# Kernel tuning notes

Hardware: AMD Instinct MI355X
Metric: run time of the kernel (lower is better)

The kernel has to match this reference:

```python
import jax, jax.numpy as jnp
import numpy as np

EPS = 1e-6
B, DIM, H, W = 2, 128, 64, 64
HEADS, DH = 4, 64            # dim_head = dim // heads * 2
INNER = HEADS * DH           # 256


def _dwsep(x, dw, pw):
    """depthwise 3x3 (groups=C, SAME) followed by 1x1 pointwise. x: [b,C,h,w]."""
    C = x.shape[1]
    y = jax.lax.conv_general_dilated(x, dw, (1, 1), 'SAME',
                                     feature_group_count=C,
                                     dimension_numbers=('NCHW', 'OIHW', 'NCHW'))
    return jnp.einsum('bchw,oc->bohw', y, pw)


def _head_ln(x, w, b):
    """per-head LayerNorm over last dim. x: [b,heads,N,dh]; w,b: [heads,dh]."""
    mu = x.mean(-1, keepdims=True)
    var = jnp.mean((x - mu) ** 2, -1, keepdims=True)
    return (x - mu) * jax.lax.rsqrt(var + EPS) * w[None, :, None, :] + b[None, :, None, :]


def setup_inputs() -> dict:
    key = jax.random.key(0)
    ks = jax.random.split(key, 8)
    s = 0.02
    return {
        'x': jax.random.normal(ks[0], (B, DIM, H, W), jnp.float32),
        'pe_w': jax.random.normal(ks[1], (DIM, 2), jnp.float32) * s,   # 1x1 conv coords->dim
        'pe_b': jnp.zeros((DIM,), jnp.float32),
        'qkv_dw': jax.random.normal(ks[2], (DIM, 1, 3, 3), jnp.float32) * s,
        'qkv_pw': jax.random.normal(ks[3], (3 * INNER, DIM), jnp.float32) * s,
        'out_dw': jax.random.normal(ks[4], (INNER, 1, 3, 3), jnp.float32) * s,
        'out_pw': jax.random.normal(ks[5], (DIM, INNER), jnp.float32) * s,
        'nq_w': jnp.ones((HEADS, DH), jnp.float32), 'nq_b': jnp.zeros((HEADS, DH), jnp.float32),
        'nk_w': jnp.ones((HEADS, DH), jnp.float32), 'nk_b': jnp.zeros((HEADS, DH), jnp.float32),
        'no_w': jnp.ones((HEADS, DH), jnp.float32), 'no_b': jnp.zeros((HEADS, DH), jnp.float32),
        'ln_w': jnp.ones((DIM,), jnp.float32), 'ln_b': jnp.zeros((DIM,), jnp.float32),
    }


def reference(x, pe_w, pe_b, qkv_dw, qkv_pw, out_dw, out_pw,
              nq_w, nq_b, nk_w, nk_b, no_w, no_b, ln_w, ln_b):
    b, c, h, w = x.shape
    heads, dh = nq_w.shape
    n = h * w

    # Euclidean positional encoding: linspace mesh [2,h,w] -> 1x1 conv -> add
    gx = jnp.linspace(0.0, 1.0, h)
    gy = jnp.linspace(0.0, 1.0, w)
    mesh = jnp.stack(jnp.meshgrid(gx, gy, indexing='ij'), 0)          # [2,h,w]
    pos = jnp.einsum('chw,dc->dhw', mesh, pe_w) + pe_b[:, None, None]
    x = x + pos[None]

    # QKV via depthwise-separable conv
    qkv = _dwsep(x, qkv_dw, qkv_pw)                                   # [b,3*inner,h,w]
    q, k, v = jnp.split(qkv, 3, axis=1)

    def to_heads(t):  # 'b (dim_head heads) h w -> b heads (h w) dim_head'
        return t.reshape(b, dh, heads, n).transpose(0, 2, 3, 1)

    q, k, v = map(to_heads, (q, k, v))                                # [b,heads,n,dh]
    q = _head_ln(q, nq_w, nq_b)
    k = _head_ln(k, nk_w, nk_b)

    attn = jnp.einsum('bhid,bhjd->bhij', q, k) * (dh ** -0.5)
    attn = jax.nn.softmax(attn, axis=-1)
    out = jnp.einsum('bhij,bhjd->bhid', attn, v)
    out = out + v                                                      # skip connection
    out = _head_ln(out, no_w, no_b)

    # 'b heads (h w) dim_head -> b (dim_head heads) h w'
    out = out.transpose(0, 3, 1, 2).reshape(b, dh * heads, h, w)
    out = _dwsep(out, out_dw, out_pw)                                  # [b,dim,h,w]

    # LayerNorm2d over channel dim at each spatial position
    mu = out.mean(1, keepdims=True)
    var = jnp.mean((out - mu) ** 2, 1, keepdims=True)
    out = (out - mu) * jax.lax.rsqrt(var + EPS)
    out = out * ln_w[None, :, None, None] + ln_b[None, :, None, None]
    return out
```

## Files before the change

kernel.cpp:

```cpp
#include <hip/hip_runtime.h>

#define BB 2
#define NTOK 4096
#define DIM 128
#define INNER 256
#define HEADS 4
#define DH 64
#define QS 0.18033688011112043f

typedef unsigned short u16;
typedef __attribute__((ext_vector_type(8))) short bf16x8;
typedef __attribute__((ext_vector_type(16))) float f32x16;

__device__ inline unsigned f2bf1(float f) {
  union { float f; unsigned u; } a; a.f = f;
  return (a.u + 0x7fffu + ((a.u >> 16) & 1u)) >> 16;
}
__device__ inline unsigned packbf(float lo, float hi) {
  return f2bf1(lo) | (f2bf1(hi) << 16);
}
__device__ inline float bf2f(u16 h) {
  union { unsigned u; float f; } a; a.u = ((unsigned)h) << 16;
  return a.f;
}
__device__ inline unsigned cvtpk(float lo, float hi) {
  unsigned r;
  asm("v_cvt_pk_bf16_f32 %0, %1, %2" : "=v"(r) : "v"(lo), "v"(hi));
  return r;
}

template <int C, bool PE>
__global__ __launch_bounds__(256) void k_dwconv(const float* __restrict__ x,
    const float* __restrict__ pew, const float* __restrict__ peb,
    const float* __restrict__ dw, u16* __restrict__ out) {
  constexpr int CG = C / 16;
  __shared__ float ld[16][640];
  int bid = blockIdx.x;
  int strip = bid & 7;
  int cg = (bid >> 3) % CG;
  int b = bid / (8 * CG);
  int r0 = strip * 8;
  int t = threadIdx.x;
#pragma unroll
  for (int c = 0; c < 16; ++c) {
    int gc = cg * 16 + c;
    const float* xb = x + ((size_t)(b * C + gc)) * NTOK;
    float s0 = 0.f, s1 = 0.f, pb = 0.f;
    if (PE) {
      s0 = pew[gc * 2] * (1.f / 63.f);
      s1 = pew[gc * 2 + 1] * (1.f / 63.f);
      pb = peb[gc];
    }
#pragma unroll
    for (int u = 0; u < 3; ++u) {
      int pos = t + 256 * u;
      if (pos < 640) {
        int rr = r0 - 1 + (pos >> 6);
        int col = pos & 63;
        float v = 0.f;
        if ((unsigned)rr < 64u) {
          v = xb[rr * 64 + col];
          if (PE) v += rr * s0 + col * s1 + pb;
        }
        ld[c][pos] = v;
      }
    }
  }
  __syncthreads();
  float accv[2][16];
#pragma unroll
  for (int c = 0; c < 16; ++c) {
    const float* wp = dw + (cg * 16 + c) * 9;
    float w0 = wp[0], w1 = wp[1], w2 = wp[2], w3 = wp[3], w4 = wp[4];
    float w5 = wp[5], w6 = wp[6], w7 = wp[7], w8 = wp[8];
#pragma unroll
    for (int pp = 0; pp < 2; ++pp) {
      int p = t + 256 * pp;
      int lr = (p >> 6) + 1;
      int j = p & 63;
      const float* rm = &ld[c][(lr - 1) * 64];
      const float* rc = &ld[c][lr * 64];
      const float* rp = &ld[c][(lr + 1) * 64];
      float acc = rm[j] * w1 + rc[j] * w4 + rp[j] * w7;
      if (j > 0)  acc += rm[j - 1] * w0 + rc[j - 1] * w3 + rp[j - 1] * w6;
      if (j < 63) acc += rm[j + 1] * w2 + rc[j + 1] * w5 + rp[j + 1] * w8;
      accv[pp][c] = acc;
    }
  }
#pragma unroll
  for (int pp = 0; pp < 2; ++pp) {
    int p = t + 256 * pp;
    unsigned ow[8];
#pragma unroll
    for (int q = 0; q < 8; ++q) ow[q] = packbf(accv[pp][2 * q], accv[pp][2 * q + 1]);
    u16* ob = out + ((size_t)(b * NTOK) + strip * 512 + p) * C + cg * 16;
    *(uint4*)(ob) = *(uint4*)&ow[0];
    *(uint4*)(ob + 8) = *(uint4*)&ow[4];
  }
}

__global__ __launch_bounds__(256) void k_gemm_qkv(
    const float* __restrict__ W, const u16* __restrict__ Yb,
    float* __restrict__ q_o, float* __restrict__ k_o, u16* __restrict__ v_t) {
  __shared__ u16 Wl[128 * 64];
  __shared__ u16 Yl[128 * 64];
  int gid = blockIdx.x;
  int nt = gid & 31;
  int mt = (gid >> 5) % 6;
  int b = gid / 192;
  int t = threadIdx.x;
  int w = t >> 6, l = t & 63;
  int wm = w >> 1, wn = w & 1;
  int hi = l >> 5, lq = l & 31;

  f32x16 acc[2][2];
#pragma unroll
  for (int fm = 0; fm < 2; ++fm)
#pragma unroll
    for (int fn = 0; fn < 2; ++fn)
#pragma unroll
      for (int r = 0; r < 16; ++r) acc[fm][fn][r] = 0.f;

  const float* Wbase = W + (size_t)(mt * 128) * 128;
  const u16* Ybase = Yb + ((size_t)(b * NTOK) + nt * 128) * 128;

  for (int k0 = 0; k0 < 128; k0 += 64) {
#pragma unroll
    for (int u = 0; u < 4; ++u) {
      int gI = t + 256 * u;
      int row = gI >> 3, g = gI & 7;
      float4 f0 = *(const float4*)(Wbase + (size_t)row * 128 + k0 + g * 8);
      float4 f1 = *(const float4*)(Wbase + (size_t)row * 128 + k0 + g * 8 + 4);
      uint4 uu;
      uu.x = cvtpk(f0.x, f0.y); uu.y = cvtpk(f0.z, f0.w);
      uu.z = cvtpk(f1.x, f1.y); uu.w = cvtpk(f1.z, f1.w);
      *(uint4*)&Wl[row * 64 + 8 * (g ^ (row & 7))] = uu;
      uint4 yv = *(const uint4*)(Ybase + (size_t)row * 128 + k0 + g * 8);
      *(uint4*)&Yl[row * 64 + 8 * (g ^ (row & 7))] = yv;
    }
    __syncthreads();
#pragma unroll
    for (int ks = 0; ks < 4; ++ks) {
      bf16x8 aF[2], bF[2];
#pragma unroll
      for (int fm = 0; fm < 2; ++fm) {
        int row = wm * 64 + fm * 32 + lq;
        aF[fm] = *(bf16x8*)&Wl[row * 64 + 8 * ((2 * ks + hi) ^ (row & 7))];
      }
#pragma unroll
      for (int fn = 0; fn < 2; ++fn) {
        int row = wn * 64 + fn * 32 + lq;
        bF[fn] = *(bf16x8*)&Yl[row * 64 + 8 * ((2 * ks + hi) ^ (row & 7))];
      }
#pragma unroll
      for (int fm = 0; fm < 2; ++fm)
#pragma unroll
        for (int fn = 0; fn < 2; ++fn)
          acc[fm][fn] = __builtin_amdgcn_mfma_f32_32x32x16_bf16(
              aF[fm], bF[fn], acc[fm][fn], 0, 0, 0);
    }
    __syncthreads();
  }

#pragma unroll
  for (int fm = 0; fm < 2; ++fm)
#pragma unroll
    for (int fn = 0; fn < 2; ++fn)
#pragma unroll
      for (int reg = 0; reg < 16; ++reg) {
        int rl = (reg & 3) + 8 * (reg >> 2) + 4 * hi;
        int o = mt * 128 + wm * 64 + fm * 32 + rl;
        int n = nt * 128 + wn * 64 + fn * 32 + lq;
        float val = acc[fm][fn][reg];
        int part = o >> 8, rr = o & 255;
        int head = rr & 3, d = rr >> 2;
        size_t idx = ((size_t)(b * HEADS + head) * DH + d) * NTOK + n;
        if (part == 0) q_o[idx] = val;
        else if (part == 1) k_o[idx] = val;
        else v_t[idx] = (u16)f2bf1(val);
      }
}

__global__ __launch_bounds__(256) void k_lnqk_t(const float* __restrict__ qh,
    const float* __restrict__ kh, u16* __restrict__ qo, u16* __restrict__ ko,
    const float* __restrict__ nqw, const float* __restrict__ nqb,
    const float* __restrict__ nkw, const float* __restrict__ nkb) {
  __shared__ float ld[64][65];
  int bh = blockIdx.x >> 6, nt = blockIdx.x & 63;
  int head = bh & 3;
  int n0 = nt * 64;
  int t = threadIdx.x;
  int dg = t & 3, nn = t >> 2;
  int dl = t >> 4, nc = t & 15;
#pragma unroll
  for (int m = 0; m < 2; ++m) {
    const float* src = (m ? kh : qh) + ((size_t)bh * DH) * NTOK + n0;
    const float* wp = (m ? nkw : nqw) + head * DH;
    const float* bp = (m ? nkb : nqb) + head * DH;
    u16* dst = (m ? ko : qo) + ((size_t)bh * NTOK + n0) * DH;
    if (m) __syncthreads();
#pragma unroll
    for (int pass = 0; pass < 4; ++pass) {
      int d = pass * 16 + dl;
      *(float4*)&ld[d][nc * 4] = *(const float4*)(src + (size_t)d * NTOK + nc * 4);
    }
    __syncthreads();
    float s1 = 0.f, s2 = 0.f;
#pragma unroll
    for (int i = 0; i < 16; ++i) {
      float v = ld[dg * 16 + i][nn];
      s1 += v; s2 += v * v;
    }
    s1 += __shfl_xor(s1, 1); s2 += __shfl_xor(s2, 1);
    s1 += __shfl_xor(s1, 2); s2 += __shfl_xor(s2, 2);
    float mu = s1 * (1.f / 64.f);
    float var = s2 * (1.f / 64.f) - mu * mu;
    float ri = rsqrtf(var + 1e-6f);
    float sc = m ? 1.f : QS;
    unsigned ow[8];
#pragma unroll
    for (int i = 0; i < 8; ++i) {
      int d0 = dg * 16 + 2 * i;
      float y0 = ((ld[d0][nn] - mu) * ri * wp[d0] + bp[d0]) * sc;
      float y1 = ((ld[d0 + 1][nn] - mu) * ri * wp[d0 + 1] + bp[d0 + 1]) * sc;
      ow[i] = packbf(y0, y1);
    }
    *(uint4*)(dst + (size_t)nn * DH + dg * 16) = *(uint4*)&ow[0];
    *(uint4*)(dst + (size_t)nn * DH + dg * 16 + 8) = *(uint4*)&ow[4];
  }
}

__global__ __launch_bounds__(512, 4) void k_attn4(
    const u16* __restrict__ qb, const u16* __restrict__ kb,
    const u16* __restrict__ vtb, const float* __restrict__ now,
    const float* __restrict__ nob, float* __restrict__ att) {
  __shared__ __align__(16) u16 kvbuf[16384];
  __shared__ float mlm[256], mll[256];
  __shared__ float nw[DH], nb[DH];
  const int bh = blockIdx.x >> 6, qt = blockIdx.x & 63;
  const int b = bh >> 2, head = bh & 3;
  const int t = threadIdx.x;
  const int w = t >> 6, l = t & 63;
  const int qg = w & 1, h = w >> 1;
  const int hi = l >> 5, lq = l & 31;
  if (t < DH) { nw[t] = now[head * DH + t]; nb[t] = nob[head * DH + t]; }

  const int q0 = qt * 64 + qg * 32;
  const u16* qrow = qb + (size_t)(bh * NTOK + q0 + lq) * DH;
  bf16x8 qf[4];
#pragma unroll
  for (int ks = 0; ks < 4; ++ks)
    qf[ks] = *(const bf16x8*)(qrow + 16 * ks + 8 * hi);

  const int st = t & 127;
  const int KQs = h * 4096, VQs = h * 4096 + 2048;
  const u16* kbase = kb + (size_t)(bh * NTOK) * DH;
  const u16* vbase = vtb + (size_t)(bh * DH) * NTOK;
  uint4 kr0, kr1, vr0, vr1;
  const int krow = st >> 3, kg = st & 7;
  const int vrow = st >> 2, vg = st & 3;

  auto loadTile = [&](int s) {
    int kv0 = h * 1024 + s * 32;
    kr0 = *(const uint4*)(kbase + (size_t)(kv0 + krow) * DH + kg * 8);
    kr1 = *(const uint4*)(kbase + (size_t)(kv0 + krow + 16) * DH + kg * 8);
    vr0 = *(const uint4*)(vbase + (size_t)vrow * NTOK + kv0 + vg * 8);
    vr1 = *(const uint4*)(vbase + (size_t)(vrow + 32) * NTOK + kv0 + vg * 8);
  };
  loadTile(0);

  f32x16 oT0, oT1;
#pragma unroll
  for (int i = 0; i < 16; ++i) { oT0[i] = 0.f; oT1[i] = 0.f; }
  float m_s = -1e30f, l_s = 0.f;
  const u16* KL = kvbuf + KQs;
  const u16* VL = kvbuf + VQs;

  for (int s = 0; s < 32; ++s) {
    __syncthreads();
    *(uint4*)&kvbuf[KQs + krow * 64 + 8 * (kg ^ (krow & 7))] = kr0;
    *(uint4*)&kvbuf[KQs + (krow + 16) * 64 + 8 * (kg ^ ((krow + 16) & 7))] = kr1;
    *(uint4*)&kvbuf[VQs + vrow * 32 + 8 * (vg ^ ((vrow >> 1) & 3))] = vr0;
    *(uint4*)&kvbuf[VQs + (vrow + 32) * 32 + 8 * (vg ^ (((vrow + 32) >> 1) & 3))] = vr1;
    __syncthreads();
    if (s < 31) loadTile(s + 1);

    f32x16 sT;
#pragma unroll
    for (int i = 0; i < 16; ++i) sT[i] = 0.f;
#pragma unroll
    for (int ks = 0; ks < 4; ++ks) {
      bf16x8 a = *(bf16x8*)&KL[lq * 64 + 8 * ((2 * ks + hi) ^ (lq & 7))];
      sT = __builtin_amdgcn_mfma_f32_32x32x16_bf16(a, qf[ks], sT, 0, 0, 0);
    }
    float mo = sT[0];
#pragma unroll
    for (int i = 1; i < 16; ++i) mo = fmaxf(mo, sT[i]);
    mo = fmaxf(mo, __shfl_xor(mo, 32));
    float mn = fmaxf(m_s, mo);
    if (!__all(mn - m_s <= 8.0f)) {
      float alpha = exp2f(m_s - mn);
      m_s = mn;
      l_s *= alpha;
#pragma unroll
      for (int i = 0; i < 16; ++i) { oT0[i] *= alpha; oT1[i] *= alpha; }
    }
    unsigned pw[8];
    float rs = 0.f;
#pragma unroll
    for (int j = 0; j < 8; ++j) {
      float e0 = exp2f(sT[2 * j] - m_s);
      float e1 = exp2f(sT[2 * j + 1] - m_s);
      rs += e0 + e1;
      pw[j] = cvtpk(e0, e1);
    }
    rs += __shfl_xor(rs, 32);
    l_s += rs;
    bf16x8 pf[2];
#pragma unroll
    for (int ks = 0; ks < 2; ++ks) {
      unsigned z0 = hi ? pw[4 * ks] : pw[4 * ks + 2];
      unsigned z1 = hi ? pw[4 * ks + 1] : pw[4 * ks + 3];
      unsigned r0 = (unsigned)__shfl_xor((int)z0, 32);
      unsigned r1 = (unsigned)__shfl_xor((int)z1, 32);
      union { unsigned u[4]; bf16x8 v; } U;
      if (hi) { U.u[0] = r0; U.u[1] = r1; U.u[2] = pw[4 * ks + 2]; U.u[3] = pw[4 * ks + 3]; }
      else    { U.u[0] = pw[4 * ks]; U.u[1] = pw[4 * ks + 1]; U.u[2] = r0; U.u[3] = r1; }
      pf[ks] = U.v;
    }
#pragma unroll
    for (int ks = 0; ks < 2; ++ks) {
      bf16x8 v0 = *(bf16x8*)&VL[lq * 32 + 8 * ((2 * ks + hi) ^ ((lq >> 1) & 3))];
      bf16x8 v1 = *(bf16x8*)&VL[(32 + lq) * 32 + 8 * ((2 * ks + hi) ^ (((32 + lq) >> 1) & 3))];
      oT0 = __builtin_amdgcn_mfma_f32_32x32x16_bf16(v0, pf[ks], oT0, 0, 0, 0);
      oT1 = __builtin_amdgcn_mfma_f32_32x32x16_bf16(v1, pf[ks], oT1, 0, 0, 0);
    }
  }

  float* mrg = (float*)kvbuf;
  __syncthreads();
  if (h >= 2) {
    float* mg = mrg + ((h - 2) * 2 + qg) * 2048;
#pragma unroll
    for (int i = 0; i < 16; ++i) {
      mg[i * 64 + l] = oT0[i];
      mg[(16 + i) * 64 + l] = oT1[i];
    }
    mlm[((h - 2) * 2 + qg) * 64 + l] = m_s;
    mll[((h - 2) * 2 + qg) * 64 + l] = l_s;
  }
  __syncthreads();
  if (h < 2) {
    int slot = h * 2 + qg;
    const float* mg = mrg + slot * 2048;
    float m1 = mlm[slot * 64 + l], l1 = mll[slot * 64 + l];
    float M = fmaxf(m_s, m1);
    float a0 = exp2f(m_s - M), a1 = exp2f(m1 - M);
#pragma unroll
    for (int i = 0; i < 16; ++i) {
      oT0[i] = oT0[i] * a0 + mg[i * 64 + l] * a1;
      oT1[i] = oT1[i] * a0 + mg[(16 + i) * 64 + l] * a1;
    }
    l_s = l_s * a0 + l1 * a1;
    m_s = M;
  }
  __syncthreads();
  if (h == 1) {
    float* mg = mrg + qg * 2048;
#pragma unroll
    for (int i = 0; i < 16; ++i) {
      mg[i * 64 + l] = oT0[i];
      mg[(16 + i) * 64 + l] = oT1[i];
    }
    mlm[qg * 64 + l] = m_s;
    mll[qg * 64 + l] = l_s;
  }
  __syncthreads();
  if (h == 0) {
    const float* mg = mrg + qg * 2048;
    float m1 = mlm[qg * 64 + l], l1 = mll[qg * 64 + l];
    float M = fmaxf(m_s, m1);
    float a0 = exp2f(m_s - M), a1 = exp2f(m1 - M);
    float L = l_s * a0 + l1 * a1;
    float inv = 1.f / L;
    float ov[32];
#pragma unroll
    for (int i = 0; i < 16; ++i) {
      ov[i] = (oT0[i] * a0 + mg[i * 64 + l] * a1) * inv;
      ov[16 + i] = (oT1[i] * a0 + mg[(16 + i) * 64 + l] * a1) * inv;
    }
    int n = q0 + lq;
#pragma unroll
    for (int dt = 0; dt < 2; ++dt)
#pragma unroll
      for (int g = 0; g < 4; ++g)
#pragma unroll
        for (int r = 0; r < 4; ++r) {
          int d = dt * 32 + g * 8 + hi * 4 + r;
          ov[dt * 16 + g * 4 + r] +=
              bf2f(vtb[((size_t)(bh * DH) + d) * NTOK + n]);
        }
    float s1 = 0.f, s2 = 0.f;
#pragma unroll
    for (int i = 0; i < 32; ++i) { s1 += ov[i]; s2 += ov[i] * ov[i]; }
    s1 += __shfl_xor(s1, 32);
    s2 += __shfl_xor(s2, 32);
    float mu = s1 * (1.f / 64.f);
    float va = s2 * (1.f / 64.f) - mu * mu;
    float ri = rsqrtf(va + 1e-6f);
    float* ob = att + (size_t)b * INNER * NTOK + n;
#pragma unroll
    for (int dt = 0; dt < 2; ++dt)
#pragma unroll
      for (int g = 0; g < 4; ++g)
#pragma unroll
        for (int r = 0; r < 4; ++r) {
          int d = dt * 32 + g * 8 + hi * 4 + r;
          float y = (ov[dt * 16 + g * 4 + r] - mu) * ri * nw[d] + nb[d];
          ob[(size_t)(d * 4 + head) * NTOK] = y;
        }
  }
}

__global__ __launch_bounds__(256) void k_gemm_ln(
    const float* __restrict__ W, const u16* __restrict__ Yb,
    const float* __restrict__ lnw, const float* __restrict__ lnb,
    float* __restrict__ out) {
  __shared__ u16 Wl[128 * 64];
  __shared__ u16 Yl[64 * 64];
  __shared__ float red[256];
  int gid = blockIdx.x;
  int nt = gid & 63;
  int b = gid >> 6;
  int t = threadIdx.x;
  int w = t >> 6, l = t & 63;
  int wm = w >> 1, wn = w & 1;
  int hi = l >> 5, lq = l & 31;

  f32x16 acc[2];
#pragma unroll
  for (int fm = 0; fm < 2; ++fm)
#pragma unroll
    for (int r = 0; r < 16; ++r) acc[fm][r] = 0.f;

  const u16* Ybase = Yb + ((size_t)(b * NTOK) + nt * 64) * INNER;

  for (int k0 = 0; k0 < 256; k0 += 64) {
#pragma unroll
    for (int u = 0; u < 4; ++u) {
      int gI = t + 256 * u;
      int row = gI >> 3, g = gI & 7;
      float4 f0 = *(const float4*)(W + (size_t)row * 256 + k0 + g * 8);
      float4 f1 = *(const float4*)(W + (size_t)row * 256 + k0 + g * 8 + 4);
      uint4 uu;
      uu.x = cvtpk(f0.x, f0.y); uu.y = cvtpk(f0.z, f0.w);
      uu.z = cvtpk(f1.x, f1.y); uu.w = cvtpk(f1.z, f1.w);
      *(uint4*)&Wl[row * 64 + 8 * (g ^ (row & 7))] = uu;
    }
#pragma unroll
    for (int u = 0; u < 2; ++u) {
      int gI = t + 256 * u;
      int row = gI >> 3, g = gI & 7;
      uint4 yv = *(const uint4*)(Ybase + (size_t)row * 256 + k0 + g * 8);
      *(uint4*)&Yl[row * 64 + 8 * (g ^ (row & 7))] = yv;
    }
    __syncthreads();
#pragma unroll
    for (int ks = 0; ks < 4; ++ks) {
      bf16x8 aF[2], bF;
#pragma unroll
      for (int fm = 0; fm < 2; ++fm) {
        int row = wm * 64 + fm * 32 + lq;
        aF[fm] = *(bf16x8*)&Wl[row * 64 + 8 * ((2 * ks + hi) ^ (row & 7))];
      }
      {
        int row = wn * 32 + lq;
        bF = *(bf16x8*)&Yl[row * 64 + 8 * ((2 * ks + hi) ^ (row & 7))];
      }
#pragma unroll
      for (int fm = 0; fm < 2; ++fm)
        acc[fm] = __builtin_amdgcn_mfma_f32_32x32x16_bf16(aF[fm], bF, acc[fm], 0, 0, 0);
    }
    __syncthreads();
  }

  float s1 = 0.f, s2 = 0.f;
#pragma unroll
  for (int fm = 0; fm < 2; ++fm)
#pragma unroll
    for (int r = 0; r < 16; ++r) {
      float v = acc[fm][r];
      s1 += v; s2 += v * v;
    }
  s1 += __shfl_xor(s1, 32);
  s2 += __shfl_xor(s2, 32);
  int col = wn * 32 + lq;
  if (hi == 0) { red[wm * 128 + col] = s1; red[wm * 128 + 64 + col] = s2; }
  __syncthreads();
  float t1 = red[col] + red[128 + col];
  float t2 = red[64 + col] + red[192 + col];
  float mu = t1 * (1.f / 128.f);
  float var = t2 * (1.f / 128.f) - mu * mu;
  float ri = rsqrtf(var + 1e-6f);
  int n = nt * 64 + col;
  float* ob = out + (size_t)b * DIM * NTOK + n;
#pragma unroll
  for (int fm = 0; fm < 2; ++fm)
#pragma unroll
    for (int r = 0; r < 16; ++r) {
      int m = wm * 64 + fm * 32 + (r & 3) + 8 * (r >> 2) + 4 * hi;
      float y = (acc[fm][r] - mu) * ri * lnw[m] + lnb[m];
      ob[(size_t)m * NTOK] = y;
    }
}

extern "C" void kernel_launch(void* const* d_in, const int* in_sizes, int n_in,
                              void* d_out, int out_size, void* d_ws,
                              size_t ws_size, hipStream_t stream) {
  const float* x      = (const float*)d_in[0];
  const float* pe_w   = (const float*)d_in[1];
  const float* pe_b   = (const float*)d_in[2];
  const float* qkv_dw = (const float*)d_in[3];
  const float* qkv_pw = (const float*)d_in[4];
  const float* out_dw = (const float*)d_in[5];
  const float* out_pw = (const float*)d_in[6];
  const float* nq_w   = (const float*)d_in[7];
  const float* nq_b   = (const float*)d_in[8];
  const float* nk_w   = (const float*)d_in[9];
  const float* nk_b   = (const float*)d_in[10];
  const float* no_w   = (const float*)d_in[11];
  const float* no_b   = (const float*)d_in[12];
  const float* ln_w   = (const float*)d_in[13];
  const float* ln_b   = (const float*)d_in[14];

  float* ws = (float*)d_ws;
  u16*   dwyb = (u16*)ws;
  float* qhb  = ws + (1u << 19);
  float* khb  = ws + (1u << 19) + (1u << 21);
  u16*   vtb  = (u16*)(ws + (1u << 19) + (2u << 21));
  u16*   qbb  = (u16*)(ws + (1u << 19) + (2u << 21) + (1u << 20));
  u16*   kbb  = (u16*)(ws + (1u << 19) + (2u << 21) + (2u << 20));
  float* att  = qhb;
  u16*   db16 = (u16*)khb;
  float* outp = (float*)d_out;

  k_dwconv<DIM, true><<<dim3(128), dim3(256), 0, stream>>>(
      x, pe_w, pe_b, qkv_dw, dwyb);
  k_gemm_qkv<<<dim3(BB * 6 * 32), dim3(256), 0, stream>>>(
      qkv_pw, dwyb, qhb, khb, vtb);
  k_lnqk_t<<<dim3(512), dim3(256), 0, stream>>>(
      qhb, khb, qbb, kbb, nq_w, nq_b, nk_w, nk_b);
  k_attn4<<<dim3(512), dim3(512), 0, stream>>>(qbb, kbb, vtb, no_w, no_b, att);
  k_dwconv<INNER, false><<<dim3(256), dim3(256), 0, stream>>>(
      att, nullptr, nullptr, out_dw, db16);
  k_gemm_ln<<<dim3(BB * 64), dim3(256), 0, stream>>>(
      out_pw, db16, ln_w, ln_b, outp);
}
```

Before: 223.3 us.

## Load attention K/V fragments directly from global and halve dwconv strips

The attention kernel no longer stages K/V tiles through shared memory with barriers. Each of the four waves loads its MFMA operands straight from global memory (through cache) for its own KV quarter, and a block now covers 32 queries with 256 threads, giving twice as many blocks. The final merge combines the three partial softmax states sequentially in wave 0. The depthwise conv kernels now process 4-row strips, doubling their grid size. This removes per-iteration syncs and LDS traffic, at the cost of uncoalesced per-lane global loads for K/V and a heavier serial merge.

```diff
diff --git a/kernel.cpp b/kernel.cpp
--- a/kernel.cpp
+++ b/kernel.cpp
@@ -34,12 +34,12 @@
     const float* __restrict__ pew, const float* __restrict__ peb,
     const float* __restrict__ dw, u16* __restrict__ out) {
   constexpr int CG = C / 16;
-  __shared__ float ld[16][640];
+  __shared__ float ld[16][384];
   int bid = blockIdx.x;
-  int strip = bid & 7;
-  int cg = (bid >> 3) % CG;
-  int b = bid / (8 * CG);
-  int r0 = strip * 8;
+  int strip = bid & 15;
+  int cg = (bid >> 4) % CG;
+  int b = bid / (16 * CG);
+  int r0 = strip * 4;
   int t = threadIdx.x;
 #pragma unroll
   for (int c = 0; c < 16; ++c) {
@@ -52,9 +52,9 @@
       pb = peb[gc];
     }
 #pragma unroll
-    for (int u = 0; u < 3; ++u) {
+    for (int u = 0; u < 2; ++u) {
       int pos = t + 256 * u;
-      if (pos < 640) {
+      if (pos < 384) {
         int rr = r0 - 1 + (pos >> 6);
         int col = pos & 63;
         float v = 0.f;
@@ -67,36 +67,26 @@
     }
   }
   __syncthreads();
-  float accv[2][16];
+  int lr = (t >> 6) + 1;
+  int j = t & 63;
+  float res[16];
 #pragma unroll
   for (int c = 0; c < 16; ++c) {
     const float* wp = dw + (cg * 16 + c) * 9;
-    float w0 = wp[0], w1 = wp[1], w2 = wp[2], w3 = wp[3], w4 = wp[4];
-    float w5 = wp[5], w6 = wp[6], w7 = wp[7], w8 = wp[8];
-#pragma unroll
-    for (int pp = 0; pp < 2; ++pp) {
-      int p = t + 256 * pp;
-      int lr = (p >> 6) + 1;
-      int j = p & 63;
-      const float* rm = &ld[c][(lr - 1) * 64];
-      const float* rc = &ld[c][lr * 64];
-      const float* rp = &ld[c][(lr + 1) * 64];
-      float acc = rm[j] * w1 + rc[j] * w4 + rp[j] * w7;
-      if (j > 0)  acc += rm[j - 1] * w0 + rc[j - 1] * w3 + rp[j - 1] * w6;
-      if (j < 63) acc += rm[j + 1] * w2 + rc[j + 1] * w5 + rp[j + 1] * w8;
-      accv[pp][c] = acc;
-    }
-  }
-#pragma unroll
-  for (int pp = 0; pp < 2; ++pp) {
-    int p = t + 256 * pp;
-    unsigned ow[8];
-#pragma unroll
-    for (int q = 0; q < 8; ++q) ow[q] = packbf(accv[pp][2 * q], accv[pp][2 * q + 1]);
-    u16* ob = out + ((size_t)(b * NTOK) + strip * 512 + p) * C + cg * 16;
-    *(uint4*)(ob) = *(uint4*)&ow[0];
-    *(uint4*)(ob + 8) = *(uint4*)&ow[4];
-  }
+    const float* rm = &ld[c][(lr - 1) * 64];
+    const float* rc = &ld[c][lr * 64];
+    const float* rp = &ld[c][(lr + 1) * 64];
+    float acc = rm[j] * wp[1] + rc[j] * wp[4] + rp[j] * wp[7];
+    if (j > 0)  acc += rm[j - 1] * wp[0] + rc[j - 1] * wp[3] + rp[j - 1] * wp[6];
+    if (j < 63) acc += rm[j + 1] * wp[2] + rc[j + 1] * wp[5] + rp[j + 1] * wp[8];
+    res[c] = acc;
+  }
+  unsigned ow[8];
+#pragma unroll
+  for (int q = 0; q < 8; ++q) ow[q] = packbf(res[2 * q], res[2 * q + 1]);
+  u16* ob = out + ((size_t)(b * NTOK) + strip * 256 + t) * C + cg * 16;
+  *(uint4*)(ob) = *(uint4*)&ow[0];
+  *(uint4*)(ob + 8) = *(uint4*)&ow[4];
 }
 
 __global__ __launch_bounds__(256) void k_gemm_qkv(
@@ -230,67 +220,43 @@
   }
 }
 
-__global__ __launch_bounds__(512, 4) void k_attn4(
+__global__ __launch_bounds__(256, 4) void k_attn5(
     const u16* __restrict__ qb, const u16* __restrict__ kb,
     const u16* __restrict__ vtb, const float* __restrict__ now,
     const float* __restrict__ nob, float* __restrict__ att) {
-  __shared__ __align__(16) u16 kvbuf[16384];
-  __shared__ float mlm[256], mll[256];
+  __shared__ float mrg[3][2048];
+  __shared__ float mstore[3][64], lstore[3][64];
   __shared__ float nw[DH], nb[DH];
-  const int bh = blockIdx.x >> 6, qt = blockIdx.x & 63;
+  const int bh = blockIdx.x >> 7, qt = blockIdx.x & 127;
   const int b = bh >> 2, head = bh & 3;
   const int t = threadIdx.x;
-  const int w = t >> 6, l = t & 63;
-  const int qg = w & 1, h = w >> 1;
+  const int h = t >> 6, l = t & 63;
   const int hi = l >> 5, lq = l & 31;
   if (t < DH) { nw[t] = now[head * DH + t]; nb[t] = nob[head * DH + t]; }
 
-  const int q0 = qt * 64 + qg * 32;
+  const int q0 = qt * 32;
   const u16* qrow = qb + (size_t)(bh * NTOK + q0 + lq) * DH;
   bf16x8 qf[4];
 #pragma unroll
   for (int ks = 0; ks < 4; ++ks)
     qf[ks] = *(const bf16x8*)(qrow + 16 * ks + 8 * hi);
 
-  const int st = t & 127;
-  const int KQs = h * 4096, VQs = h * 4096 + 2048;
-  const u16* kbase = kb + (size_t)(bh * NTOK) * DH;
-  const u16* vbase = vtb + (size_t)(bh * DH) * NTOK;
-  uint4 kr0, kr1, vr0, vr1;
-  const int krow = st >> 3, kg = st & 7;
-  const int vrow = st >> 2, vg = st & 3;
-
-  auto loadTile = [&](int s) {
-    int kv0 = h * 1024 + s * 32;
-    kr0 = *(const uint4*)(kbase + (size_t)(kv0 + krow) * DH + kg * 8);
-    kr1 = *(const uint4*)(kbase + (size_t)(kv0 + krow + 16) * DH + kg * 8);
-    vr0 = *(const uint4*)(vbase + (size_t)vrow * NTOK + kv0 + vg * 8);
-    vr1 = *(const uint4*)(vbase + (size_t)(vrow + 32) * NTOK + kv0 + vg * 8);
-  };
-  loadTile(0);
+  const u16* krow = kb + ((size_t)(bh * NTOK) + h * 1024 + lq) * DH;
+  const u16* vrow0 = vtb + ((size_t)(bh * DH) + lq) * NTOK + h * 1024;
+  const u16* vrow1 = vtb + ((size_t)(bh * DH) + 32 + lq) * NTOK + h * 1024;
 
   f32x16 oT0, oT1;
 #pragma unroll
   for (int i = 0; i < 16; ++i) { oT0[i] = 0.f; oT1[i] = 0.f; }
   float m_s = -1e30f, l_s = 0.f;
-  const u16* KL = kvbuf + KQs;
-  const u16* VL = kvbuf + VQs;
 
   for (int s = 0; s < 32; ++s) {
-    __syncthreads();
-    *(uint4*)&kvbuf[KQs + krow * 64 + 8 * (kg ^ (krow & 7))] = kr0;
-    *(uint4*)&kvbuf[KQs + (krow + 16) * 64 + 8 * (kg ^ ((krow + 16) & 7))] = kr1;
-    *(uint4*)&kvbuf[VQs + vrow * 32 + 8 * (vg ^ ((vrow >> 1) & 3))] = vr0;
-    *(uint4*)&kvbuf[VQs + (vrow + 32) * 32 + 8 * (vg ^ (((vrow + 32) >> 1) & 3))] = vr1;
-    __syncthreads();
-    if (s < 31) loadTile(s + 1);
-
     f32x16 sT;
 #pragma unroll
     for (int i = 0; i < 16; ++i) sT[i] = 0.f;
 #pragma unroll
     for (int ks = 0; ks < 4; ++ks) {
-      bf16x8 a = *(bf16x8*)&KL[lq * 64 + 8 * ((2 * ks + hi) ^ (lq & 7))];
+      bf16x8 a = *(const bf16x8*)(krow + (size_t)s * 32 * DH + 16 * ks + 8 * hi);
       sT = __builtin_amdgcn_mfma_f32_32x32x16_bf16(a, qf[ks], sT, 0, 0, 0);
     }
     float mo = sT[0];
@@ -330,65 +296,43 @@
     }
 #pragma unroll
     for (int ks = 0; ks < 2; ++ks) {
-      bf16x8 v0 = *(bf16x8*)&VL[lq * 32 + 8 * ((2 * ks + hi) ^ ((lq >> 1) & 3))];
-      bf16x8 v1 = *(bf16x8*)&VL[(32 + lq) * 32 + 8 * ((2 * ks + hi) ^ (((32 + lq) >> 1) & 3))];
+      bf16x8 v0 = *(const bf16x8*)(vrow0 + s * 32 + 16 * ks + 8 * hi);
+      bf16x8 v1 = *(const bf16x8*)(vrow1 + s * 32 + 16 * ks + 8 * hi);
       oT0 = __builtin_amdgcn_mfma_f32_32x32x16_bf16(v0, pf[ks], oT0, 0, 0, 0);
       oT1 = __builtin_amdgcn_mfma_f32_32x32x16_bf16(v1, pf[ks], oT1, 0, 0, 0);
     }
   }
 
-  float* mrg = (float*)kvbuf;
   __syncthreads();
-  if (h >= 2) {
-    float* mg = mrg + ((h - 2) * 2 + qg) * 2048;
+  if (h > 0) {
+    float* mg = mrg[h - 1];
 #pragma unroll
     for (int i = 0; i < 16; ++i) {
       mg[i * 64 + l] = oT0[i];
       mg[(16 + i) * 64 + l] = oT1[i];
     }
-    mlm[((h - 2) * 2 + qg) * 64 + l] = m_s;
-    mll[((h - 2) * 2 + qg) * 64 + l] = l_s;
-  }
-  __syncthreads();
-  if (h < 2) {
-    int slot = h * 2 + qg;
-    const float* mg = mrg + slot * 2048;
-    float m1 = mlm[slot * 64 + l], l1 = mll[slot * 64 + l];
-    float M = fmaxf(m_s, m1);
-    float a0 = exp2f(m_s - M), a1 = exp2f(m1 - M);
-#pragma unroll
-    for (int i = 0; i < 16; ++i) {
-      oT0[i] = oT0[i] * a0 + mg[i * 64 + l] * a1;
-      oT1[i] = oT1[i] * a0 + mg[(16 + i) * 64 + l] * a1;
-    }
-    l_s = l_s * a0 + l1 * a1;
-    m_s = M;
-  }
-  __syncthreads();
-  if (h == 1) {
-    float* mg = mrg + qg * 2048;
-#pragma unroll
-    for (int i = 0; i < 16; ++i) {
-      mg[i * 64 + l] = oT0[i];
-      mg[(16 + i) * 64 + l] = oT1[i];
-    }
-    mlm[qg * 64 + l] = m_s;
-    mll[qg * 64 + l] = l_s;
+    mstore[h - 1][l] = m_s;
+    lstore[h - 1][l] = l_s;
   }
   __syncthreads();
   if (h == 0) {
-    const float* mg = mrg + qg * 2048;
-    float m1 = mlm[qg * 64 + l], l1 = mll[qg * 64 + l];
-    float M = fmaxf(m_s, m1);
-    float a0 = exp2f(m_s - M), a1 = exp2f(m1 - M);
-    float L = l_s * a0 + l1 * a1;
-    float inv = 1.f / L;
     float ov[32];
 #pragma unroll
-    for (int i = 0; i < 16; ++i) {
-      ov[i] = (oT0[i] * a0 + mg[i * 64 + l] * a1) * inv;
-      ov[16 + i] = (oT1[i] * a0 + mg[(16 + i) * 64 + l] * a1) * inv;
-    }
+    for (int i = 0; i < 16; ++i) { ov[i] = oT0[i]; ov[16 + i] = oT1[i]; }
+#pragma unroll
+    for (int hp = 0; hp < 3; ++hp) {
+      float m1 = mstore[hp][l], l1 = lstore[hp][l];
+      const float* mg = mrg[hp];
+      float M = fmaxf(m_s, m1);
+      float a0 = exp2f(m_s - M), a1 = exp2f(m1 - M);
+#pragma unroll
+      for (int i = 0; i < 32; ++i) ov[i] = ov[i] * a0 + mg[i * 64 + l] * a1;
+      l_s = l_s * a0 + l1 * a1;
+      m_s = M;
+    }
+    float inv = 1.f / l_s;
+#pragma unroll
+    for (int i = 0; i < 32; ++i) ov[i] *= inv;
     int n = q0 + lq;
 #pragma unroll
     for (int dt = 0; dt < 2; ++dt)
@@ -544,14 +488,14 @@
   u16*   db16 = (u16*)khb;
   float* outp = (float*)d_out;
 
-  k_dwconv<DIM, true><<<dim3(128), dim3(256), 0, stream>>>(
+  k_dwconv<DIM, true><<<dim3(256), dim3(256), 0, stream>>>(
       x, pe_w, pe_b, qkv_dw, dwyb);
   k_gemm_qkv<<<dim3(BB * 6 * 32), dim3(256), 0, stream>>>(
       qkv_pw, dwyb, qhb, khb, vtb);
   k_lnqk_t<<<dim3(512), dim3(256), 0, stream>>>(
       qhb, khb, qbb, kbb, nq_w, nq_b, nk_w, nk_b);
-  k_attn4<<<dim3(512), dim3(512), 0, stream>>>(qbb, kbb, vtb, no_w, no_b, att);
-  k_dwconv<INNER, false><<<dim3(256), dim3(256), 0, stream>>>(
+  k_attn5<<<dim3(1024), dim3(256), 0, stream>>>(qbb, kbb, vtb, no_w, no_b, att);
+  k_dwconv<INNER, false><<<dim3(512), dim3(256), 0, stream>>>(
       att, nullptr, nullptr, out_dw, db16);
   k_gemm_ln<<<dim3(BB * 64), dim3(256), 0, stream>>>(
       out_pw, db16, ln_w, ln_b, outp);
```

New measurement: 267.2 us. 19.6% more time.
